# Kernel optimization log

Hardware: AMD Instinct MI355X
Metric: run time of the kernel (lower is better)

## Reference

```python
import jax, jax.numpy as jnp
import numpy as np

N = 100000
E = 3200000
NFEAT = 256
NHID = 128
NCLASS = 40
SCALE = 1.0


def setup_inputs() -> dict:
    key = jax.random.key(0)
    ks = jax.random.split(key, 8)
    x = jax.random.normal(ks[0], (N, NFEAT), dtype=jnp.float32)
    adj_row = jnp.sort(jax.random.randint(ks[1], (E,), 0, N, dtype=jnp.int32))
    adj_col = jax.random.randint(ks[2], (E,), 0, N, dtype=jnp.int32)
    adj_val = jax.random.uniform(ks[3], (E,), dtype=jnp.float32)
    # parameters (reset_parameters: weight ~ N(0,1), bias ~ N(-1,1) -> normal with mean -1? no:
    # bias.normal_(-stdv, stdv) with stdv=1 means mean=-1, std=1)
    W1 = jax.random.normal(ks[4], (NFEAT, NHID), dtype=jnp.float32)
    b1 = jax.random.normal(ks[5], (NHID,), dtype=jnp.float32) - 1.0
    W2 = jax.random.normal(ks[6], (NHID, NCLASS), dtype=jnp.float32)
    b2 = jax.random.normal(ks[7], (NCLASS,), dtype=jnp.float32) - 1.0
    return {"x": x, "adj_row": adj_row, "adj_col": adj_col, "adj_val": adj_val,
            "i": 0, "W1": W1, "b1": b1, "W2": W2, "b2": b2}


def spmm(row, col, val, dense):
    # adj @ dense where adj is sparse COO [N, N]
    gathered = val[:, None] * dense[col]          # [E, D]
    return jax.ops.segment_sum(gathered, row, num_segments=N)


def reference(x, adj_row, adj_col, adj_val, i, W1, b1, W2, b2):
    # layer 1: support = x @ W1; out = adj @ support + b1
    h = spmm(adj_row, adj_col, adj_val, x @ W1) + b1
    h = jax.nn.relu(h) * SCALE
    # dropout is identity (eval mode / training=False)
    # layer 2
    logits = spmm(adj_row, adj_col, adj_val, h @ W2) + b2
    return jax.nn.log_softmax(logits, axis=1)
```

## Files before the change

kernel.cpp:

```cpp
#include <hip/hip_runtime.h>
#include <hip/hip_bf16.h>
#include <math.h>


#define GCN_NFEAT 256
#define GCN_NHID  128
#define GCN_NCLASS 40

typedef __bf16 bf16_t;
typedef bf16_t bf16x8 __attribute__((ext_vector_type(8)));
typedef float  f32x4  __attribute__((ext_vector_type(4)));

static __device__ __forceinline__ unsigned short f2b(float f) {
    bf16_t b = (bf16_t)f;
    return *(unsigned short*)&b;
}
static __device__ __forceinline__ float blo(unsigned int u) {
    return __uint_as_float(u << 16);
}
static __device__ __forceinline__ float bhi(unsigned int u) {
    return __uint_as_float(u & 0xffff0000u);
}

__global__ __launch_bounds__(256) void k_row_ptr(
    const int* __restrict__ row, int* __restrict__ row_ptr, int n_rows, int n_edges)
{
    int r = blockIdx.x * blockDim.x + threadIdx.x;
    if (r > n_rows) return;
    int lo = 0, hi = n_edges;
    while (lo < hi) {
        int mid = (lo + hi) >> 1;
        if (row[mid] < r) lo = mid + 1; else hi = mid;
    }
    row_ptr[r] = lo;
}

__global__ __launch_bounds__(256) void k_prep_w1t(
    const float* __restrict__ w1, bf16_t* __restrict__ w1t)
{
    int idx = blockIdx.x * 256 + threadIdx.x;
    int c = idx & 127;
    int k = idx >> 7;
    w1t[(size_t)c * GCN_NFEAT + k] = (bf16_t)w1[(size_t)k * GCN_NHID + c];
}

__global__ __launch_bounds__(256) void k_prep_w2t(
    const float* __restrict__ w2, bf16_t* __restrict__ w2t)
{
    int idx = blockIdx.x * 256 + threadIdx.x;
    if (idx >= 48 * GCN_NHID) return;
    int c = idx / GCN_NHID;
    int k = idx - c * GCN_NHID;
    float v = (c < GCN_NCLASS) ? w2[(size_t)k * GCN_NCLASS + c] : 0.f;
    w2t[idx] = (bf16_t)v;
}

__global__ __launch_bounds__(256) void k_gemm1(
    const float* __restrict__ x, const bf16_t* __restrict__ w1t,
    bf16_t* __restrict__ out, int nrows)
{
    __shared__ __align__(16) bf16_t As[128][72];
    __shared__ __align__(16) bf16_t Bs[128][72];

    const int tid  = threadIdx.x;
    const int wave = tid >> 6, lane = tid & 63;
    const int wm = wave >> 1, wn = wave & 1;
    const int lm = lane & 15, quad = lane >> 4;
    const int r0 = blockIdx.x * 128;

    f32x4 acc[4][4] = {};

    for (int k0 = 0; k0 < GCN_NFEAT; k0 += 64) {
        {
            const int row = tid >> 1, half = tid & 1;
            const int gr = r0 + row;
            union { bf16_t b[32]; uint4 q[4]; } t;
            if (gr < nrows) {
                const float* p = x + (size_t)gr * GCN_NFEAT + k0 + half * 32;
#pragma unroll
                for (int i = 0; i < 8; i++) {
                    float4 v = ((const float4*)p)[i];
                    t.b[i*4+0] = (bf16_t)v.x; t.b[i*4+1] = (bf16_t)v.y;
                    t.b[i*4+2] = (bf16_t)v.z; t.b[i*4+3] = (bf16_t)v.w;
                }
            } else {
#pragma unroll
                for (int i = 0; i < 4; i++) t.q[i] = make_uint4(0,0,0,0);
            }
            uint4* dst = (uint4*)&As[row][half * 32];
#pragma unroll
            for (int i = 0; i < 4; i++) dst[i] = t.q[i];
        }
        {
            const int colc = tid >> 1, half = tid & 1;
            const uint4* src = (const uint4*)(w1t + (size_t)colc * GCN_NFEAT + k0 + half * 32);
            uint4* dst = (uint4*)&Bs[colc][half * 32];
#pragma unroll
            for (int i = 0; i < 4; i++) dst[i] = src[i];
        }
        __syncthreads();

#pragma unroll
        for (int ks = 0; ks < 2; ks++) {
            bf16x8 af[4], bfr[4];
#pragma unroll
            for (int i = 0; i < 4; i++)
                af[i] = *(const bf16x8*)&As[wm*64 + i*16 + lm][ks*32 + quad*8];
#pragma unroll
            for (int j = 0; j < 4; j++)
                bfr[j] = *(const bf16x8*)&Bs[wn*64 + j*16 + lm][ks*32 + quad*8];
#pragma unroll
            for (int i = 0; i < 4; i++)
#pragma unroll
                for (int j = 0; j < 4; j++)
                    acc[i][j] = __builtin_amdgcn_mfma_f32_16x16x32_bf16(
                        af[i], bfr[j], acc[i][j], 0, 0, 0);
        }
        __syncthreads();
    }

#pragma unroll
    for (int i = 0; i < 4; i++) {
#pragma unroll
        for (int reg = 0; reg < 4; reg++) {
            const int gr = r0 + wm*64 + i*16 + quad*4 + reg;
            if (gr < nrows) {
#pragma unroll
                for (int j = 0; j < 4; j++) {
                    const int gc = wn*64 + j*16 + lm;
                    out[(size_t)gr * GCN_NHID + gc] = (bf16_t)acc[i][j][reg];
                }
            }
        }
    }
}

__global__ __launch_bounds__(256) void k_spmm1(
    const int* __restrict__ row_ptr, const int* __restrict__ col,
    const float* __restrict__ val, const unsigned int* __restrict__ sup,
    const float* __restrict__ b1, unsigned int* __restrict__ h, int nrows)
{
    const int wid  = (blockIdx.x * blockDim.x + threadIdx.x) >> 6;
    const int lane = threadIdx.x & 63;
    if (wid >= nrows) return;
    const int e0 = row_ptr[wid];
    const int e1 = row_ptr[wid + 1];
    const int sub = lane & 15;

    float ax = 0.f, ay = 0.f;
    int e = e0;
    for (; e + 16 <= e1; e += 16) {
        const int   cv = col[e + sub];
        const float vv = val[e + sub];
#pragma unroll
        for (int j = 0; j < 16; j++) {
            const int   cj = __shfl(cv, j, 64);
            const float vj = __shfl(vv, j, 64);
            const unsigned int u = sup[(unsigned)(cj << 6) + lane];
            ax = fmaf(vj, blo(u), ax);
            ay = fmaf(vj, bhi(u), ay);
        }
    }
    for (; e < e1; e++) {
        const int c = col[e];
        const float v = val[e];
        const unsigned int u = sup[(unsigned)(c << 6) + lane];
        ax = fmaf(v, blo(u), ax);
        ay = fmaf(v, bhi(u), ay);
    }

    const float2 bb = *(const float2*)(b1 + lane * 2);
    const float ox = fmaxf(ax + bb.x, 0.f);
    const float oy = fmaxf(ay + bb.y, 0.f);
    h[(unsigned)(wid << 6) + lane] = (unsigned int)f2b(ox) | ((unsigned int)f2b(oy) << 16);
}

__global__ __launch_bounds__(256) void k_gemm2(
    const bf16_t* __restrict__ h, const bf16_t* __restrict__ w2t,
    bf16_t* __restrict__ out, int nrows)
{
    __shared__ __align__(16) bf16_t As[128][136];
    __shared__ __align__(16) bf16_t Bs[48][136];

    const int tid  = threadIdx.x;
    const int wave = tid >> 6, lane = tid & 63;
    const int lm = lane & 15, quad = lane >> 4;
    const int r0 = blockIdx.x * 128;

    {
        const int row = tid >> 1, half = tid & 1;
        const int gr = r0 + row;
        uint4* dst = (uint4*)&As[row][half * 64];
        if (gr < nrows) {
            const uint4* src = (const uint4*)(h + (size_t)gr * GCN_NHID + half * 64);
#pragma unroll
            for (int i = 0; i < 8; i++) dst[i] = src[i];
        } else {
#pragma unroll
            for (int i = 0; i < 8; i++) dst[i] = make_uint4(0,0,0,0);
        }
    }
    for (int idx = tid; idx < 48 * 16; idx += 256) {
        const int c = idx >> 4, seg = idx & 15;
        ((uint4*)&Bs[c][0])[seg] = ((const uint4*)(w2t + (size_t)c * GCN_NHID))[seg];
    }
    __syncthreads();

    f32x4 acc[2][3] = {};
#pragma unroll
    for (int ks = 0; ks < 4; ks++) {
        bf16x8 af[2], bfr[3];
#pragma unroll
        for (int i = 0; i < 2; i++)
            af[i] = *(const bf16x8*)&As[wave*32 + i*16 + lm][ks*32 + quad*8];
#pragma unroll
        for (int j = 0; j < 3; j++)
            bfr[j] = *(const bf16x8*)&Bs[j*16 + lm][ks*32 + quad*8];
#pragma unroll
        for (int i = 0; i < 2; i++)
#pragma unroll
            for (int j = 0; j < 3; j++)
                acc[i][j] = __builtin_amdgcn_mfma_f32_16x16x32_bf16(
                    af[i], bfr[j], acc[i][j], 0, 0, 0);
    }

#pragma unroll
    for (int i = 0; i < 2; i++) {
#pragma unroll
        for (int reg = 0; reg < 4; reg++) {
            const int gr = r0 + wave*32 + i*16 + quad*4 + reg;
            if (gr < nrows) {
#pragma unroll
                for (int j = 0; j < 3; j++) {
                    const int gc = j*16 + lm;
                    if (gc < GCN_NCLASS)
                        out[(size_t)gr * GCN_NCLASS + gc] = (bf16_t)acc[i][j][reg];
                }
            }
        }
    }
}

__global__ __launch_bounds__(256) void k_spmm2_lsm(
    const int* __restrict__ row_ptr, const int* __restrict__ col,
    const float* __restrict__ val, const unsigned int* __restrict__ sup2,
    const float* __restrict__ b2, float* __restrict__ out, int nrows)
{
    const int wid  = (blockIdx.x * blockDim.x + threadIdx.x) >> 6;
    const int lane = threadIdx.x & 63;
    const int g    = lane / 20;
    const int li   = lane - g * 20;
    const int r    = wid * 3 + g;
    const bool active = (g < 3) && (r < nrows);

    int e0 = 0, e1 = 0;
    if (active) { e0 = row_ptr[r]; e1 = row_ptr[r + 1]; }

    float ax = 0.f, ay = 0.f;
    int e = e0;
    for (; e + 3 < e1; e += 4) {
        const int c0 = col[e],   c1 = col[e+1], c2 = col[e+2], c3 = col[e+3];
        const float v0 = val[e], v1 = val[e+1], v2 = val[e+2], v3 = val[e+3];
        const unsigned int u0 = sup2[(unsigned)(c0 * 20) + li];
        const unsigned int u1 = sup2[(unsigned)(c1 * 20) + li];
        const unsigned int u2 = sup2[(unsigned)(c2 * 20) + li];
        const unsigned int u3 = sup2[(unsigned)(c3 * 20) + li];
        ax = fmaf(v0, blo(u0), ax); ay = fmaf(v0, bhi(u0), ay);
        ax = fmaf(v1, blo(u1), ax); ay = fmaf(v1, bhi(u1), ay);
        ax = fmaf(v2, blo(u2), ax); ay = fmaf(v2, bhi(u2), ay);
        ax = fmaf(v3, blo(u3), ax); ay = fmaf(v3, bhi(u3), ay);
    }
    for (; e < e1; e++) {
        const unsigned int u = sup2[(unsigned)(col[e] * 20) + li];
        const float v = val[e];
        ax = fmaf(v, blo(u), ax); ay = fmaf(v, bhi(u), ay);
    }

    float l0 = -INFINITY, l1 = -INFINITY;
    if (active) {
        l0 = ax + b2[li * 2];
        l1 = ay + b2[li * 2 + 1];
    }

    float m = fmaxf(l0, l1);
#pragma unroll
    for (int off = 16; off >= 1; off >>= 1) {
        const float t = __shfl_down(m, off, 64);
        if (li + off < 20) m = fmaxf(m, t);
    }
    m = __shfl(m, g * 20, 64);

    float s = active ? (__expf(l0 - m) + __expf(l1 - m)) : 0.f;
#pragma unroll
    for (int off = 16; off >= 1; off >>= 1) {
        const float t = __shfl_down(s, off, 64);
        if (li + off < 20) s += t;
    }
    s = __shfl(s, g * 20, 64);

    if (active) {
        const float lse = m + __logf(s);
        float* p = out + (size_t)r * GCN_NCLASS + li * 2;
        p[0] = l0 - lse;
        p[1] = l1 - lse;
    }
}

extern "C" void kernel_launch(void* const* d_in, const int* in_sizes, int n_in,
                              void* d_out, int out_size, void* d_ws, size_t ws_size,
                              hipStream_t stream)
{
    const float* x       = (const float*)d_in[0];
    const int*   adj_row = (const int*)  d_in[1];
    const int*   adj_col = (const int*)  d_in[2];
    const float* adj_val = (const float*)d_in[3];
    const float* W1 = (const float*)d_in[5];
    const float* b1 = (const float*)d_in[6];
    const float* W2 = (const float*)d_in[7];
    const float* b2 = (const float*)d_in[8];
    float* out = (float*)d_out;

    const int N = in_sizes[0] / GCN_NFEAT;
    const int E = in_sizes[1];

    char* ws = (char*)d_ws;
    size_t off = 0;
    int* row_ptr = (int*)(ws + off);
    off += (((size_t)(N + 1) * sizeof(int)) + 1023) & ~(size_t)1023;
    bf16_t* w1t = (bf16_t*)(ws + off);
    off += ((size_t)GCN_NHID * GCN_NFEAT * 2 + 1023) & ~(size_t)1023;
    bf16_t* w2t = (bf16_t*)(ws + off);
    off += ((size_t)48 * GCN_NHID * 2 + 1023) & ~(size_t)1023;
    bf16_t* sup1 = (bf16_t*)(ws + off);
    off += ((size_t)N * GCN_NHID * 2 + 1023) & ~(size_t)1023;
    bf16_t* h = (bf16_t*)(ws + off);
    bf16_t* sup2 = sup1;

    k_row_ptr<<<(N + 1 + 255) / 256, 256, 0, stream>>>(adj_row, row_ptr, N, E);
    k_prep_w1t<<<GCN_NHID * GCN_NFEAT / 256, 256, 0, stream>>>(W1, w1t);
    k_prep_w2t<<<(48 * GCN_NHID + 255) / 256, 256, 0, stream>>>(W2, w2t);
    k_gemm1<<<(N + 127) / 128, 256, 0, stream>>>(x, w1t, sup1, N);
    k_spmm1<<<(N + 3) / 4, 256, 0, stream>>>(row_ptr, adj_col, adj_val,
                                             (const unsigned int*)sup1, b1,
                                             (unsigned int*)h, N);
    k_gemm2<<<(N + 127) / 128, 256, 0, stream>>>(h, w2t, sup2, N);
    const int nw2 = (N + 2) / 3;
    k_spmm2_lsm<<<(nw2 + 3) / 4, 256, 0, stream>>>(row_ptr, adj_col, adj_val,
                                                   (const unsigned int*)sup2, b2, out, N);
}
```

Baseline: 417.3 us.

## Software-pipeline SpMM gathers and pad second-layer support rows to 64

Layer-1 SpMM now uses wave-uniform row bounds and double-buffers batches of 8 column/value loads and feature gathers, so the next batch's loads are in flight while the current batch is accumulated. Inline asm fences keep the compiler from interleaving waits into the load bursts. The layer-2 support matrix is stored with a padded leading dimension of 64 bf16 so rows are 128-byte aligned and indexed with shifts, and its SpMM unrolls to 8 outstanding gathers. This costs more registers per wave and writes some unused padding columns.

```diff
diff --git a/kernel.cpp b/kernel.cpp
--- a/kernel.cpp
+++ b/kernel.cpp
@@ -6,6 +6,7 @@
 #define GCN_NFEAT 256
 #define GCN_NHID  128
 #define GCN_NCLASS 40
+#define SUP2_LD   64
 
 typedef __bf16 bf16_t;
 typedef bf16_t bf16x8 __attribute__((ext_vector_type(8)));
@@ -135,38 +136,75 @@
     }
 }
 
+#define SPMM1_LOADCV(CS, VS, B)                                          \
+    _Pragma("unroll")                                                    \
+    for (int j = 0; j < 8; j++) {                                        \
+        int gi = e0 + (B) + j;                                           \
+        if (gi > emax) gi = emax;                                        \
+        CS[j] = col[gi];                                                 \
+        VS[j] = ((B) + j < n) ? val[gi] : 0.f;                           \
+    }
+
+#define SPMM1_ISSUE(U, CS)                                               \
+    _Pragma("unroll")                                                    \
+    for (int j = 0; j < 8; j++) {                                        \
+        const unsigned int* p = sup + ((size_t)(unsigned)CS[j] << 6);    \
+        U[j] = p[lane];                                                  \
+    }
+
+#define SPMM1_FENCE(U)                                                   \
+    asm volatile("" : "+v"(U[0]), "+v"(U[1]), "+v"(U[2]), "+v"(U[3]),    \
+                      "+v"(U[4]), "+v"(U[5]), "+v"(U[6]), "+v"(U[7]));
+
+#define SPMM1_FMA(U, VS)                                                 \
+    _Pragma("unroll")                                                    \
+    for (int j = 0; j < 8; j++) {                                        \
+        ax = fmaf(VS[j], blo(U[j]), ax);                                 \
+        ay = fmaf(VS[j], bhi(U[j]), ay);                                 \
+    }
+
 __global__ __launch_bounds__(256) void k_spmm1(
     const int* __restrict__ row_ptr, const int* __restrict__ col,
     const float* __restrict__ val, const unsigned int* __restrict__ sup,
-    const float* __restrict__ b1, unsigned int* __restrict__ h, int nrows)
+    const float* __restrict__ b1, unsigned int* __restrict__ h,
+    int nrows, int n_edges)
 {
     const int wid  = (blockIdx.x * blockDim.x + threadIdx.x) >> 6;
     const int lane = threadIdx.x & 63;
     if (wid >= nrows) return;
-    const int e0 = row_ptr[wid];
-    const int e1 = row_ptr[wid + 1];
-    const int sub = lane & 15;
+    const int e0   = __builtin_amdgcn_readfirstlane(row_ptr[wid]);
+    const int e1   = __builtin_amdgcn_readfirstlane(row_ptr[wid + 1]);
+    const int n    = e1 - e0;
+    const int emax = n_edges - 1;
 
     float ax = 0.f, ay = 0.f;
-    int e = e0;
-    for (; e + 16 <= e1; e += 16) {
-        const int   cv = col[e + sub];
-        const float vv = val[e + sub];
-#pragma unroll
-        for (int j = 0; j < 16; j++) {
-            const int   cj = __shfl(cv, j, 64);
-            const float vj = __shfl(vv, j, 64);
-            const unsigned int u = sup[(unsigned)(cj << 6) + lane];
-            ax = fmaf(vj, blo(u), ax);
-            ay = fmaf(vj, bhi(u), ay);
-        }
-    }
-    for (; e < e1; e++) {
-        const int c = col[e];
-        const float v = val[e];
-        const unsigned int u = sup[(unsigned)(c << 6) + lane];
-        ax = fmaf(v, blo(u), ax);
-        ay = fmaf(v, bhi(u), ay);
+
+    if (n > 0) {
+        int   csA[8], csB[8];
+        float vsA[8], vsB[8];
+        unsigned uA[8], uB[8];
+
+        SPMM1_LOADCV(csA, vsA, 0)
+        SPMM1_ISSUE(uA, csA)
+        int base = 0;
+        while (true) {
+            if (base + 8 < n) {
+                SPMM1_LOADCV(csB, vsB, base + 8)
+                SPMM1_ISSUE(uB, csB)
+            }
+            SPMM1_FENCE(uA)
+            SPMM1_FMA(uA, vsA)
+            base += 8;
+            if (base >= n) break;
+            if (base + 8 < n) {
+                SPMM1_LOADCV(csA, vsA, base + 8)
+                SPMM1_ISSUE(uA, csA)
+            }
+            SPMM1_FENCE(uB)
+            SPMM1_FMA(uB, vsB)
+            base += 8;
+            if (base >= n) break;
+        }
     }
 
     const float2 bb = *(const float2*)(b1 + lane * 2);
@@ -233,8 +271,7 @@
 #pragma unroll
                 for (int j = 0; j < 3; j++) {
                     const int gc = j*16 + lm;
-                    if (gc < GCN_NCLASS)
-                        out[(size_t)gr * GCN_NCLASS + gc] = (bf16_t)acc[i][j][reg];
+                    out[(size_t)gr * SUP2_LD + gc] = (bf16_t)acc[i][j][reg];
                 }
             }
         }
@@ -258,20 +295,45 @@
 
     float ax = 0.f, ay = 0.f;
     int e = e0;
-    for (; e + 3 < e1; e += 4) {
+    for (; e + 7 < e1; e += 8) {
         const int c0 = col[e],   c1 = col[e+1], c2 = col[e+2], c3 = col[e+3];
-        const float v0 = val[e], v1 = val[e+1], v2 = val[e+2], v3 = val[e+3];
-        const unsigned int u0 = sup2[(unsigned)(c0 * 20) + li];
-        const unsigned int u1 = sup2[(unsigned)(c1 * 20) + li];
-        const unsigned int u2 = sup2[(unsigned)(c2 * 20) + li];
-        const unsigned int u3 = sup2[(unsigned)(c3 * 20) + li];
+        const int c4 = col[e+4], c5 = col[e+5], c6 = col[e+6], c7 = col[e+7];
+        const float v0 = val[e],   v1 = val[e+1], v2 = val[e+2], v3 = val[e+3];
+        const float v4 = val[e+4], v5 = val[e+5], v6 = val[e+6], v7 = val[e+7];
+        unsigned int u0 = sup2[((unsigned)c0 << 5) + li];
+        unsigned int u1 = sup2[((unsigned)c1 << 5) + li];
+        unsigned int u2 = sup2[((unsigned)c2 << 5) + li];
+        unsigned int u3 = sup2[((unsigned)c3 << 5) + li];
+        unsigned int u4 = sup2[((unsigned)c4 << 5) + li];
+        unsigned int u5 = sup2[((unsigned)c5 << 5) + li];
+        unsigned int u6 = sup2[((unsigned)c6 << 5) + li];
+        unsigned int u7 = sup2[((unsigned)c7 << 5) + li];
+        asm volatile("" : "+v"(u0), "+v"(u1), "+v"(u2), "+v"(u3),
+                          "+v"(u4), "+v"(u5), "+v"(u6), "+v"(u7));
         ax = fmaf(v0, blo(u0), ax); ay = fmaf(v0, bhi(u0), ay);
         ax = fmaf(v1, blo(u1), ax); ay = fmaf(v1, bhi(u1), ay);
         ax = fmaf(v2, blo(u2), ax); ay = fmaf(v2, bhi(u2), ay);
         ax = fmaf(v3, blo(u3), ax); ay = fmaf(v3, bhi(u3), ay);
+        ax = fmaf(v4, blo(u4), ax); ay = fmaf(v4, bhi(u4), ay);
+        ax = fmaf(v5, blo(u5), ax); ay = fmaf(v5, bhi(u5), ay);
+        ax = fmaf(v6, blo(u6), ax); ay = fmaf(v6, bhi(u6), ay);
+        ax = fmaf(v7, blo(u7), ax); ay = fmaf(v7, bhi(u7), ay);
+    }
+    for (; e + 3 < e1; e += 4) {
+        const int c0 = col[e],   c1 = col[e+1], c2 = col[e+2], c3 = col[e+3];
+        const float v0 = val[e], v1 = val[e+1], v2 = val[e+2], v3 = val[e+3];
+        unsigned int u0 = sup2[((unsigned)c0 << 5) + li];
+        unsigned int u1 = sup2[((unsigned)c1 << 5) + li];
+        unsigned int u2 = sup2[((unsigned)c2 << 5) + li];
+        unsigned int u3 = sup2[((unsigned)c3 << 5) + li];
+        asm volatile("" : "+v"(u0), "+v"(u1), "+v"(u2), "+v"(u3));
+        ax = fmaf(v0, blo(u0), ax); ay = fmaf(v0, bhi(u0), ay);
+        ax = fmaf(v1, blo(u1), ax); ay = fmaf(v1, bhi(u1), ay);
+        ax = fmaf(v2, blo(u2), ax); ay = fmaf(v2, bhi(u2), ay);
+        ax = fmaf(v3, blo(u3), ax); ay = fmaf(v3, bhi(u3), ay);
     }
     for (; e < e1; e++) {
-        const unsigned int u = sup2[(unsigned)(col[e] * 20) + li];
+        const unsigned int u = sup2[((unsigned)col[e] << 5) + li];
         const float v = val[e];
         ax = fmaf(v, blo(u), ax); ay = fmaf(v, bhi(u), ay);
     }
@@ -342,7 +404,7 @@
     k_gemm1<<<(N + 127) / 128, 256, 0, stream>>>(x, w1t, sup1, N);
     k_spmm1<<<(N + 3) / 4, 256, 0, stream>>>(row_ptr, adj_col, adj_val,
                                              (const unsigned int*)sup1, b1,
-                                             (unsigned int*)h, N);
+                                             (unsigned int*)h, N, E);
     k_gemm2<<<(N + 127) / 128, 256, 0, stream>>>(h, w2t, sup2, N);
     const int nw2 = (N + 2) / 3;
     k_spmm2_lsm<<<(nw2 + 3) / 4, 256, 0, stream>>>(row_ptr, adj_col, adj_val,
```

New measurement: 419.1 us. Within noise of the previous version (+0.4%).

## Split each row's edges across four lane groups with vector gathers in both SpMMs

Applied to the files above, without the earlier changes.

Both SpMM kernels now have each wave's four 16-lane quarters process different edges of the same row. Each lane gathers a 16-byte (layer 1) or 8-byte (layer 2) chunk of the neighbour's feature row, and the partial sums are combined with xor shuffles. Layer-2 support is stored padded to a 64-element stride so each row's gathers are aligned, and spmm2 moves from three rows per wave to one row per wave. The aim is more memory-level parallelism and fewer, wider loads per edge. The cost is the cross-lane reduction, more work on the tail, and extra padding written in gemm2.

```diff
diff --git a/kernel.cpp b/kernel.cpp
--- a/kernel.cpp
+++ b/kernel.cpp
@@ -6,6 +6,7 @@
 #define GCN_NFEAT 256
 #define GCN_NHID  128
 #define GCN_NCLASS 40
+#define SUP2_LD   64
 
 typedef __bf16 bf16_t;
 typedef bf16_t bf16x8 __attribute__((ext_vector_type(8)));
@@ -135,44 +136,101 @@
     }
 }
 
+#define S1_FENCE(U) asm volatile("" : "+v"(U.x), "+v"(U.y), "+v"(U.z), "+v"(U.w));
+#define S1_FMA(U, V)                                   \
+    a0 = fmaf(V, blo(U.x), a0); a1 = fmaf(V, bhi(U.x), a1); \
+    a2 = fmaf(V, blo(U.y), a2); a3 = fmaf(V, bhi(U.y), a3); \
+    a4 = fmaf(V, blo(U.z), a4); a5 = fmaf(V, bhi(U.z), a5); \
+    a6 = fmaf(V, blo(U.w), a6); a7 = fmaf(V, bhi(U.w), a7);
+
 __global__ __launch_bounds__(256) void k_spmm1(
     const int* __restrict__ row_ptr, const int* __restrict__ col,
-    const float* __restrict__ val, const unsigned int* __restrict__ sup,
+    const float* __restrict__ val, const bf16_t* __restrict__ sup,
     const float* __restrict__ b1, unsigned int* __restrict__ h, int nrows)
 {
     const int wid  = (blockIdx.x * blockDim.x + threadIdx.x) >> 6;
     const int lane = threadIdx.x & 63;
     if (wid >= nrows) return;
-    const int e0 = row_ptr[wid];
-    const int e1 = row_ptr[wid + 1];
-    const int sub = lane & 15;
-
-    float ax = 0.f, ay = 0.f;
-    int e = e0;
-    for (; e + 16 <= e1; e += 16) {
-        const int   cv = col[e + sub];
-        const float vv = val[e + sub];
-#pragma unroll
-        for (int j = 0; j < 16; j++) {
-            const int   cj = __shfl(cv, j, 64);
-            const float vj = __shfl(vv, j, 64);
-            const unsigned int u = sup[(unsigned)(cj << 6) + lane];
-            ax = fmaf(vj, blo(u), ax);
-            ay = fmaf(vj, bhi(u), ay);
-        }
-    }
-    for (; e < e1; e++) {
-        const int c = col[e];
-        const float v = val[e];
-        const unsigned int u = sup[(unsigned)(c << 6) + lane];
-        ax = fmaf(v, blo(u), ax);
-        ay = fmaf(v, bhi(u), ay);
-    }
-
-    const float2 bb = *(const float2*)(b1 + lane * 2);
-    const float ox = fmaxf(ax + bb.x, 0.f);
-    const float oy = fmaxf(ay + bb.y, 0.f);
-    h[(unsigned)(wid << 6) + lane] = (unsigned int)f2b(ox) | ((unsigned int)f2b(oy) << 16);
+    const int q = lane >> 4;
+    const int f = lane & 15;
+    const int e0 = __builtin_amdgcn_readfirstlane(row_ptr[wid]);
+    const int e1 = __builtin_amdgcn_readfirstlane(row_ptr[wid + 1]);
+    const int n  = e1 - e0;
+    const char* supb = (const char*)sup;
+    const int fo = f * 16;
+
+    float a0=0.f,a1=0.f,a2=0.f,a3=0.f,a4=0.f,a5=0.f,a6=0.f,a7=0.f;
+
+    int base = 0;
+    for (; base + 16 <= n; base += 16) {
+        const int i0 = e0 + base + q;
+        const int   c0 = col[i0];      const float v0 = val[i0];
+        const int   c1 = col[i0 + 4];  const float v1 = val[i0 + 4];
+        const int   c2 = col[i0 + 8];  const float v2 = val[i0 + 8];
+        const int   c3 = col[i0 + 12]; const float v3 = val[i0 + 12];
+        uint4 u0 = *(const uint4*)(supb + (((size_t)(unsigned)c0) << 8) + fo);
+        uint4 u1 = *(const uint4*)(supb + (((size_t)(unsigned)c1) << 8) + fo);
+        uint4 u2 = *(const uint4*)(supb + (((size_t)(unsigned)c2) << 8) + fo);
+        uint4 u3 = *(const uint4*)(supb + (((size_t)(unsigned)c3) << 8) + fo);
+        S1_FENCE(u0) S1_FMA(u0, v0)
+        S1_FENCE(u1) S1_FMA(u1, v1)
+        S1_FENCE(u2) S1_FMA(u2, v2)
+        S1_FENCE(u3) S1_FMA(u3, v3)
+    }
+    const int rem = n - base;
+    if (rem > 0) {
+        const int elast = e1 - 1;
+        uint4 t0, t1, t2, t3;
+        float w0 = 0.f, w1 = 0.f, w2 = 0.f, w3 = 0.f;
+        {
+            int gi = e0 + base + q; if (gi > elast) gi = elast;
+            const int c = col[gi]; w0 = (q < rem) ? val[gi] : 0.f;
+            t0 = *(const uint4*)(supb + (((size_t)(unsigned)c) << 8) + fo);
+        }
+        if (rem > 4) {
+            int gi = e0 + base + 4 + q; if (gi > elast) gi = elast;
+            const int c = col[gi]; w1 = (4 + q < rem) ? val[gi] : 0.f;
+            t1 = *(const uint4*)(supb + (((size_t)(unsigned)c) << 8) + fo);
+        }
+        if (rem > 8) {
+            int gi = e0 + base + 8 + q; if (gi > elast) gi = elast;
+            const int c = col[gi]; w2 = (8 + q < rem) ? val[gi] : 0.f;
+            t2 = *(const uint4*)(supb + (((size_t)(unsigned)c) << 8) + fo);
+        }
+        if (rem > 12) {
+            int gi = e0 + base + 12 + q; if (gi > elast) gi = elast;
+            const int c = col[gi]; w3 = (12 + q < rem) ? val[gi] : 0.f;
+            t3 = *(const uint4*)(supb + (((size_t)(unsigned)c) << 8) + fo);
+        }
+        { S1_FENCE(t0) S1_FMA(t0, w0) }
+        if (rem > 4)  { S1_FENCE(t1) S1_FMA(t1, w1) }
+        if (rem > 8)  { S1_FENCE(t2) S1_FMA(t2, w2) }
+        if (rem > 12) { S1_FENCE(t3) S1_FMA(t3, w3) }
+    }
+
+    a0 += __shfl_xor(a0, 16, 64); a1 += __shfl_xor(a1, 16, 64);
+    a2 += __shfl_xor(a2, 16, 64); a3 += __shfl_xor(a3, 16, 64);
+    a4 += __shfl_xor(a4, 16, 64); a5 += __shfl_xor(a5, 16, 64);
+    a6 += __shfl_xor(a6, 16, 64); a7 += __shfl_xor(a7, 16, 64);
+    a0 += __shfl_xor(a0, 32, 64); a1 += __shfl_xor(a1, 32, 64);
+    a2 += __shfl_xor(a2, 32, 64); a3 += __shfl_xor(a3, 32, 64);
+    a4 += __shfl_xor(a4, 32, 64); a5 += __shfl_xor(a5, 32, 64);
+    a6 += __shfl_xor(a6, 32, 64); a7 += __shfl_xor(a7, 32, 64);
+
+    if (q == 0) {
+        const float4 ba = *(const float4*)(b1 + f * 8);
+        const float4 bc = *(const float4*)(b1 + f * 8 + 4);
+        const float o0 = fmaxf(a0 + ba.x, 0.f), o1 = fmaxf(a1 + ba.y, 0.f);
+        const float o2 = fmaxf(a2 + ba.z, 0.f), o3 = fmaxf(a3 + ba.w, 0.f);
+        const float o4 = fmaxf(a4 + bc.x, 0.f), o5 = fmaxf(a5 + bc.y, 0.f);
+        const float o6 = fmaxf(a6 + bc.z, 0.f), o7 = fmaxf(a7 + bc.w, 0.f);
+        uint4 pk;
+        pk.x = (unsigned)f2b(o0) | ((unsigned)f2b(o1) << 16);
+        pk.y = (unsigned)f2b(o2) | ((unsigned)f2b(o3) << 16);
+        pk.z = (unsigned)f2b(o4) | ((unsigned)f2b(o5) << 16);
+        pk.w = (unsigned)f2b(o6) | ((unsigned)f2b(o7) << 16);
+        *(uint4*)(h + ((unsigned)wid << 6) + (f << 2)) = pk;
+    }
 }
 
 __global__ __launch_bounds__(256) void k_gemm2(
@@ -233,76 +291,110 @@
 #pragma unroll
                 for (int j = 0; j < 3; j++) {
                     const int gc = j*16 + lm;
-                    if (gc < GCN_NCLASS)
-                        out[(size_t)gr * GCN_NCLASS + gc] = (bf16_t)acc[i][j][reg];
+                    out[(size_t)gr * SUP2_LD + gc] = (bf16_t)acc[i][j][reg];
                 }
+                out[(size_t)gr * SUP2_LD + 48 + lm] = (bf16_t)0.f;
             }
         }
     }
 }
+
+#define S2_FENCE(U) asm volatile("" : "+v"(U.x), "+v"(U.y));
+#define S2_FMA(U, V)                                   \
+    a0 = fmaf(V, blo(U.x), a0); a1 = fmaf(V, bhi(U.x), a1); \
+    a2 = fmaf(V, blo(U.y), a2); a3 = fmaf(V, bhi(U.y), a3);
 
 __global__ __launch_bounds__(256) void k_spmm2_lsm(
     const int* __restrict__ row_ptr, const int* __restrict__ col,
-    const float* __restrict__ val, const unsigned int* __restrict__ sup2,
+    const float* __restrict__ val, const bf16_t* __restrict__ sup2,
     const float* __restrict__ b2, float* __restrict__ out, int nrows)
 {
     const int wid  = (blockIdx.x * blockDim.x + threadIdx.x) >> 6;
     const int lane = threadIdx.x & 63;
-    const int g    = lane / 20;
-    const int li   = lane - g * 20;
-    const int r    = wid * 3 + g;
-    const bool active = (g < 3) && (r < nrows);
-
-    int e0 = 0, e1 = 0;
-    if (active) { e0 = row_ptr[r]; e1 = row_ptr[r + 1]; }
-
-    float ax = 0.f, ay = 0.f;
-    int e = e0;
-    for (; e + 3 < e1; e += 4) {
-        const int c0 = col[e],   c1 = col[e+1], c2 = col[e+2], c3 = col[e+3];
-        const float v0 = val[e], v1 = val[e+1], v2 = val[e+2], v3 = val[e+3];
-        const unsigned int u0 = sup2[(unsigned)(c0 * 20) + li];
-        const unsigned int u1 = sup2[(unsigned)(c1 * 20) + li];
-        const unsigned int u2 = sup2[(unsigned)(c2 * 20) + li];
-        const unsigned int u3 = sup2[(unsigned)(c3 * 20) + li];
-        ax = fmaf(v0, blo(u0), ax); ay = fmaf(v0, bhi(u0), ay);
-        ax = fmaf(v1, blo(u1), ax); ay = fmaf(v1, bhi(u1), ay);
-        ax = fmaf(v2, blo(u2), ax); ay = fmaf(v2, bhi(u2), ay);
-        ax = fmaf(v3, blo(u3), ax); ay = fmaf(v3, bhi(u3), ay);
-    }
-    for (; e < e1; e++) {
-        const unsigned int u = sup2[(unsigned)(col[e] * 20) + li];
-        const float v = val[e];
-        ax = fmaf(v, blo(u), ax); ay = fmaf(v, bhi(u), ay);
-    }
-
-    float l0 = -INFINITY, l1 = -INFINITY;
-    if (active) {
-        l0 = ax + b2[li * 2];
-        l1 = ay + b2[li * 2 + 1];
-    }
-
-    float m = fmaxf(l0, l1);
-#pragma unroll
-    for (int off = 16; off >= 1; off >>= 1) {
-        const float t = __shfl_down(m, off, 64);
-        if (li + off < 20) m = fmaxf(m, t);
-    }
-    m = __shfl(m, g * 20, 64);
-
-    float s = active ? (__expf(l0 - m) + __expf(l1 - m)) : 0.f;
-#pragma unroll
-    for (int off = 16; off >= 1; off >>= 1) {
-        const float t = __shfl_down(s, off, 64);
-        if (li + off < 20) s += t;
-    }
-    s = __shfl(s, g * 20, 64);
-
-    if (active) {
+    if (wid >= nrows) return;
+    const int q = lane >> 4;
+    const int f = lane & 15;
+    const int e0 = __builtin_amdgcn_readfirstlane(row_ptr[wid]);
+    const int e1 = __builtin_amdgcn_readfirstlane(row_ptr[wid + 1]);
+    const int n  = e1 - e0;
+    const char* supb = (const char*)sup2;
+    const int fo = f * 8;
+
+    float a0=0.f,a1=0.f,a2=0.f,a3=0.f;
+
+    int base = 0;
+    for (; base + 16 <= n; base += 16) {
+        const int i0 = e0 + base + q;
+        const int   c0 = col[i0];      const float v0 = val[i0];
+        const int   c1 = col[i0 + 4];  const float v1 = val[i0 + 4];
+        const int   c2 = col[i0 + 8];  const float v2 = val[i0 + 8];
+        const int   c3 = col[i0 + 12]; const float v3 = val[i0 + 12];
+        uint2 u0 = *(const uint2*)(supb + (((size_t)(unsigned)c0) << 7) + fo);
+        uint2 u1 = *(const uint2*)(supb + (((size_t)(unsigned)c1) << 7) + fo);
+        uint2 u2 = *(const uint2*)(supb + (((size_t)(unsigned)c2) << 7) + fo);
+        uint2 u3 = *(const uint2*)(supb + (((size_t)(unsigned)c3) << 7) + fo);
+        S2_FENCE(u0) S2_FMA(u0, v0)
+        S2_FENCE(u1) S2_FMA(u1, v1)
+        S2_FENCE(u2) S2_FMA(u2, v2)
+        S2_FENCE(u3) S2_FMA(u3, v3)
+    }
+    const int rem = n - base;
+    if (rem > 0) {
+        const int elast = e1 - 1;
+        uint2 t0, t1, t2, t3;
+        float w0 = 0.f, w1 = 0.f, w2 = 0.f, w3 = 0.f;
+        {
+            int gi = e0 + base + q; if (gi > elast) gi = elast;
+            const int c = col[gi]; w0 = (q < rem) ? val[gi] : 0.f;
+            t0 = *(const uint2*)(supb + (((size_t)(unsigned)c) << 7) + fo);
+        }
+        if (rem > 4) {
+            int gi = e0 + base + 4 + q; if (gi > elast) gi = elast;
+            const int c = col[gi]; w1 = (4 + q < rem) ? val[gi] : 0.f;
+            t1 = *(const uint2*)(supb + (((size_t)(unsigned)c) << 7) + fo);
+        }
+        if (rem > 8) {
+            int gi = e0 + base + 8 + q; if (gi > elast) gi = elast;
+            const int c = col[gi]; w2 = (8 + q < rem) ? val[gi] : 0.f;
+            t2 = *(const uint2*)(supb + (((size_t)(unsigned)c) << 7) + fo);
+        }
+        if (rem > 12) {
+            int gi = e0 + base + 12 + q; if (gi > elast) gi = elast;
+            const int c = col[gi]; w3 = (12 + q < rem) ? val[gi] : 0.f;
+            t3 = *(const uint2*)(supb + (((size_t)(unsigned)c) << 7) + fo);
+        }
+        { S2_FENCE(t0) S2_FMA(t0, w0) }
+        if (rem > 4)  { S2_FENCE(t1) S2_FMA(t1, w1) }
+        if (rem > 8)  { S2_FENCE(t2) S2_FMA(t2, w2) }
+        if (rem > 12) { S2_FENCE(t3) S2_FMA(t3, w3) }
+    }
+
+    a0 += __shfl_xor(a0, 16, 64); a1 += __shfl_xor(a1, 16, 64);
+    a2 += __shfl_xor(a2, 16, 64); a3 += __shfl_xor(a3, 16, 64);
+    a0 += __shfl_xor(a0, 32, 64); a1 += __shfl_xor(a1, 32, 64);
+    a2 += __shfl_xor(a2, 32, 64); a3 += __shfl_xor(a3, 32, 64);
+
+    const bool av = (f < 10);
+    float l0 = -INFINITY, l1 = -INFINITY, l2 = -INFINITY, l3 = -INFINITY;
+    if (av) {
+        const float4 bb = *(const float4*)(b2 + f * 4);
+        l0 = a0 + bb.x; l1 = a1 + bb.y; l2 = a2 + bb.z; l3 = a3 + bb.w;
+    }
+    float m = fmaxf(fmaxf(l0, l1), fmaxf(l2, l3));
+    m = fmaxf(m, __shfl_xor(m, 1, 64));
+    m = fmaxf(m, __shfl_xor(m, 2, 64));
+    m = fmaxf(m, __shfl_xor(m, 4, 64));
+    m = fmaxf(m, __shfl_xor(m, 8, 64));
+    float s = av ? (__expf(l0 - m) + __expf(l1 - m) + __expf(l2 - m) + __expf(l3 - m)) : 0.f;
+    s += __shfl_xor(s, 1, 64);
+    s += __shfl_xor(s, 2, 64);
+    s += __shfl_xor(s, 4, 64);
+    s += __shfl_xor(s, 8, 64);
+
+    if (av && q == 0) {
         const float lse = m + __logf(s);
-        float* p = out + (size_t)r * GCN_NCLASS + li * 2;
-        p[0] = l0 - lse;
-        p[1] = l1 - lse;
+        float4 o; o.x = l0 - lse; o.y = l1 - lse; o.z = l2 - lse; o.w = l3 - lse;
+        *(float4*)(out + (size_t)wid * GCN_NCLASS + f * 4) = o;
     }
 }
 
@@ -341,10 +433,8 @@
     k_prep_w2t<<<(48 * GCN_NHID + 255) / 256, 256, 0, stream>>>(W2, w2t);
     k_gemm1<<<(N + 127) / 128, 256, 0, stream>>>(x, w1t, sup1, N);
     k_spmm1<<<(N + 3) / 4, 256, 0, stream>>>(row_ptr, adj_col, adj_val,
-                                             (const unsigned int*)sup1, b1,
-                                             (unsigned int*)h, N);
+                                             sup1, b1, (unsigned int*)h, N);
     k_gemm2<<<(N + 127) / 128, 256, 0, stream>>>(h, w2t, sup2, N);
-    const int nw2 = (N + 2) / 3;
-    k_spmm2_lsm<<<(nw2 + 3) / 4, 256, 0, stream>>>(row_ptr, adj_col, adj_val,
-                                                   (const unsigned int*)sup2, b2, out, N);
-}
+    k_spmm2_lsm<<<(N + 3) / 4, 256, 0, stream>>>(row_ptr, adj_col, adj_val,
+                                                 sup2, b2, out, N);
+}
```

After: 392.9 us. -5.8%, faster.
